# Performance work log

Hardware: AMD Instinct MI355X
Metric: run time of the kernel (lower is better)

## Reference

```python
import jax, jax.numpy as jnp
import numpy as np

N_QUERY, N_BACKGND, DIM = 2048, 8192, 32


def setup_inputs() -> dict:
    key = jax.random.key(0)
    k0, k1, k2, k3 = jax.random.split(key, 4)
    x_backgnd = jax.random.normal(k0, (N_BACKGND, DIM), dtype=jnp.float32)
    y_backgnd = jax.random.normal(k1, (N_BACKGND,), dtype=jnp.float32)
    x_query = jax.random.normal(k2, (N_QUERY, DIM), dtype=jnp.float32)
    r = jax.random.uniform(k3, (N_QUERY, N_BACKGND), dtype=jnp.float32)
    sigma = jnp.array([0.1], dtype=jnp.float32)      # nn.Parameter init_sigma
    r_scale = jnp.array([3.0], dtype=jnp.float32)    # nn.Parameter init_r_scale
    w = jnp.ones((DIM,), dtype=jnp.float32)          # trainable weights matrix
    return {"x_backgnd": x_backgnd, "y_backgnd": y_backgnd, "x_query": x_query,
            "r": r, "sigma": sigma, "r_scale": r_scale, "w": w}


def reference(x_backgnd, y_backgnd, x_query, r, sigma, r_scale, w):
    # weighted Euclidean distance: ||(xq - xb) * w|| via the expansion trick,
    # avoiding the (n_query, n_backgnd, dim) difference tensor.
    xq = x_query * w           # (nq, d)
    xb = x_backgnd * w         # (nb, d)
    q2 = jnp.sum(xq * xq, axis=1, keepdims=True)        # (nq, 1)
    b2 = jnp.sum(xb * xb, axis=1)                        # (nb,)
    d2 = q2 + b2[None, :] - 2.0 * (xq @ xb.T)            # (nq, nb)
    dists = jnp.sqrt(jnp.maximum(d2, 0.0))
    # exp kernel with relationship bias, normalize, weighted sum
    k_vals = jnp.exp(-dists / sigma + r_scale * r)       # sigma, r_scale broadcast (1,)
    k_sum = jnp.sum(k_vals, axis=1, keepdims=True) + 1e-8
    weights = k_vals / k_sum
    y_pred = weights @ y_backgnd                          # (nq,)
    return y_pred
```

## Files before the change

### kernel.cpp

```cpp
#include <hip/hip_runtime.h>
#include <math.h>

#define NQ 2048
#define NB 8192
#define DIM 32

#define LOG2E 1.44269504088896340736f

typedef _Float16 half8 __attribute__((ext_vector_type(8)));
typedef float    f32x4 __attribute__((ext_vector_type(4)));

#define WS_ACC 0
#define WS_Q2  16448
#define WS_B2  24640
#define WS_XQH 57408
#define WS_XBH 188480

__global__ __launch_bounds__(256) void relnw_pre(
    const float* __restrict__ xq, const float* __restrict__ xb,
    const float* __restrict__ w,
    _Float16* __restrict__ XQh, _Float16* __restrict__ XBh,
    float* __restrict__ q2, float* __restrict__ b2,
    float* __restrict__ acc)
{
    const int tid = threadIdx.x;
    const int gi  = blockIdx.x * 256 + tid;
    if (gi < 2 * NQ) acc[gi] = 0.f;

    const int row = blockIdx.x * 64 + (tid >> 2);
    const int p   = tid & 3;
    if (row >= NQ + NB) return;

    const float* src; _Float16* dst; float* s2; float scale;
    if (row < NQ) { src = xq + (size_t)row * DIM;
                    dst = XQh + (size_t)row * DIM; s2 = q2 + row; scale = 1.f; }
    else          { int j = row - NQ;
                    src = xb + (size_t)j * DIM;
                    dst = XBh + (size_t)j * DIM;   s2 = b2 + j;   scale = -2.f; }

    const float4 xa  = ((const float4*)src)[p * 2];
    const float4 xbv = ((const float4*)src)[p * 2 + 1];
    const float4 wa  = ((const float4*)w)[p * 2];
    const float4 wb  = ((const float4*)w)[p * 2 + 1];
    const float xs[8]  = {xa.x, xa.y, xa.z, xa.w, xbv.x, xbv.y, xbv.z, xbv.w};
    const float ws_[8] = {wa.x, wa.y, wa.z, wa.w, wb.x, wb.y, wb.z, wb.w};

    half8 h;
    float s = 0.f;
#pragma unroll
    for (int c = 0; c < 8; ++c) {
        float t = xs[c] * ws_[c];
        _Float16 hh = (_Float16)t;
        float th = (float)hh;
        s = fmaf(th, th, s);
        h[c] = (_Float16)(th * scale);
    }
    *(half8*)(dst + p * 8) = h;

    s += __shfl_xor(s, 1, 64);
    s += __shfl_xor(s, 2, 64);
    if (p == 0) *s2 = s;
}

#define BT_PER_WAVE 16
#define BG_PER_WAVE (BT_PER_WAVE * 16)

__global__ __launch_bounds__(256) void relnw_main(
    const _Float16* __restrict__ XQh,
    const _Float16* __restrict__ XBh,
    const float* __restrict__ q2,
    const float* __restrict__ b2,
    const float* __restrict__ yb,
    const float* __restrict__ r,
    const float* __restrict__ sigma,
    const float* __restrict__ rscale,
    float* __restrict__ acc)
{
    const int tid  = threadIdx.x;
    const int lane = tid & 63;
    const int wid  = tid >> 6;
    const int m    = lane & 15;
    const int quad = lane >> 4;

    const int q0     = blockIdx.y * 16;
    const int bstart = (blockIdx.x * 4 + wid) * BG_PER_WAVE;

    const float c1 = -LOG2E / sigma[0];
    const float c2 =  LOG2E * rscale[0];

    const half8 afrag = *(const half8*)(XQh + (size_t)(q0 + m) * DIM + quad * 8);

    float q2r[4];
#pragma unroll
    for (int g = 0; g < 4; ++g) q2r[g] = q2[q0 + quad * 4 + g];

    const _Float16* xbp = XBh + (size_t)(bstart + m) * DIM + quad * 8;
    const float*    rp  = r + (size_t)(q0 + quad * 4) * NB + bstart + m;

    float sk[4]  = {0.f, 0.f, 0.f, 0.f};
    float sky[4] = {0.f, 0.f, 0.f, 0.f};

#pragma unroll
    for (int it = 0; it < BT_PER_WAVE; ++it) {
        const int bc = bstart + it * 16 + m;
        const half8 bfrag = *(const half8*)(xbp + (size_t)it * 16 * DIM);
        const float yv  = yb[bc];
        const float b2v = b2[bc];
        float rr[4];
#pragma unroll
        for (int g = 0; g < 4; ++g) rr[g] = rp[(size_t)g * NB + it * 16];

        f32x4 cin;
#pragma unroll
        for (int g = 0; g < 4; ++g) cin[g] = q2r[g] + b2v;

        f32x4 d2v = __builtin_amdgcn_mfma_f32_16x16x32_f16(
            afrag, bfrag, cin, 0, 0, 0);

#pragma unroll
        for (int g = 0; g < 4; ++g) {
            float d2 = fmaxf(d2v[g], 0.f);
            float dist = __builtin_amdgcn_sqrtf(d2);
            float e = fmaf(dist, c1, rr[g] * c2);
            float k = __builtin_amdgcn_exp2f(e);
            sk[g] += k;
            sky[g] = fmaf(k, yv, sky[g]);
        }
    }

#pragma unroll
    for (int off = 1; off <= 8; off <<= 1) {
#pragma unroll
        for (int g = 0; g < 4; ++g) {
            sk[g]  += __shfl_xor(sk[g],  off, 64);
            sky[g] += __shfl_xor(sky[g], off, 64);
        }
    }
    if (m == 0) {
#pragma unroll
        for (int g = 0; g < 4; ++g) {
            atomicAdd(acc + (q0 + quad * 4 + g),      sk[g]);
            atomicAdd(acc + NQ + (q0 + quad * 4 + g), sky[g]);
        }
    }
}

__global__ __launch_bounds__(256) void relnw_finalize(
    const float* __restrict__ acc, float* __restrict__ out)
{
    int q = blockIdx.x * 256 + threadIdx.x;
    if (q < NQ)
        out[q] = acc[NQ + q] / (acc[q] + 1e-8f);
}

extern "C" void kernel_launch(void* const* d_in, const int* in_sizes, int n_in,
                              void* d_out, int out_size, void* d_ws, size_t ws_size,
                              hipStream_t stream) {
    const float* xb     = (const float*)d_in[0];
    const float* yb     = (const float*)d_in[1];
    const float* xq     = (const float*)d_in[2];
    const float* r      = (const float*)d_in[3];
    const float* sigma  = (const float*)d_in[4];
    const float* rscale = (const float*)d_in[5];
    const float* w      = (const float*)d_in[6];
    float* out = (float*)d_out;

    char* ws = (char*)d_ws;
    float*    acc = (float*)(ws + WS_ACC);
    float*    q2  = (float*)(ws + WS_Q2);
    float*    b2  = (float*)(ws + WS_B2);
    _Float16* XQh = (_Float16*)(ws + WS_XQH);
    _Float16* XBh = (_Float16*)(ws + WS_XBH);

    relnw_pre<<<(NQ + NB) / 64, 256, 0, stream>>>(xq, xb, w, XQh, XBh, q2, b2, acc);

    dim3 grid(NB / (4 * BG_PER_WAVE), NQ / 16);
    relnw_main<<<grid, 256, 0, stream>>>(XQh, XBh, q2, b2, yb, r, sigma, rscale, acc);

    relnw_finalize<<<(NQ + 255) / 256, 256, 0, stream>>>(acc, out);
}
```

Before: 112.8 us.

## Fuse preprocessing into main kernel and replace atomics with per-chunk partials

Removes the separate preprocessing kernel: the main kernel now reads fp32 query/background rows directly, applies the weights, converts to fp16 and computes the squared norms in-kernel, with b2 staged in shared memory. Global atomics are replaced by per-chunk partial sums written to the workspace and reduced in the finalize kernel, which also removes the need to zero the accumulator. This saves one launch and the fp16 workspace round trip, but every block recomputes background norms and reads fp32 background data (twice the bytes of fp16) redundantly across the 128 query blocks.

```diff
diff --git a/kernel.cpp b/kernel.cpp
--- a/kernel.cpp
+++ b/kernel.cpp
@@ -10,72 +10,26 @@
 typedef _Float16 half8 __attribute__((ext_vector_type(8)));
 typedef float    f32x4 __attribute__((ext_vector_type(4)));
 
-#define WS_ACC 0
-#define WS_Q2  16448
-#define WS_B2  24640
-#define WS_XQH 57408
-#define WS_XBH 188480
-
-__global__ __launch_bounds__(256) void relnw_pre(
-    const float* __restrict__ xq, const float* __restrict__ xb,
-    const float* __restrict__ w,
-    _Float16* __restrict__ XQh, _Float16* __restrict__ XBh,
-    float* __restrict__ q2, float* __restrict__ b2,
-    float* __restrict__ acc)
-{
-    const int tid = threadIdx.x;
-    const int gi  = blockIdx.x * 256 + tid;
-    if (gi < 2 * NQ) acc[gi] = 0.f;
-
-    const int row = blockIdx.x * 64 + (tid >> 2);
-    const int p   = tid & 3;
-    if (row >= NQ + NB) return;
-
-    const float* src; _Float16* dst; float* s2; float scale;
-    if (row < NQ) { src = xq + (size_t)row * DIM;
-                    dst = XQh + (size_t)row * DIM; s2 = q2 + row; scale = 1.f; }
-    else          { int j = row - NQ;
-                    src = xb + (size_t)j * DIM;
-                    dst = XBh + (size_t)j * DIM;   s2 = b2 + j;   scale = -2.f; }
-
-    const float4 xa  = ((const float4*)src)[p * 2];
-    const float4 xbv = ((const float4*)src)[p * 2 + 1];
-    const float4 wa  = ((const float4*)w)[p * 2];
-    const float4 wb  = ((const float4*)w)[p * 2 + 1];
-    const float xs[8]  = {xa.x, xa.y, xa.z, xa.w, xbv.x, xbv.y, xbv.z, xbv.w};
-    const float ws_[8] = {wa.x, wa.y, wa.z, wa.w, wb.x, wb.y, wb.z, wb.w};
-
-    half8 h;
-    float s = 0.f;
-#pragma unroll
-    for (int c = 0; c < 8; ++c) {
-        float t = xs[c] * ws_[c];
-        _Float16 hh = (_Float16)t;
-        float th = (float)hh;
-        s = fmaf(th, th, s);
-        h[c] = (_Float16)(th * scale);
-    }
-    *(half8*)(dst + p * 8) = h;
-
-    s += __shfl_xor(s, 1, 64);
-    s += __shfl_xor(s, 2, 64);
-    if (p == 0) *s2 = s;
-}
+#define NCHUNK 32
+#define WS_PSK  0
+#define WS_PSKY (NCHUNK * NQ * 4)
 
 #define BT_PER_WAVE 16
 #define BG_PER_WAVE (BT_PER_WAVE * 16)
 
 __global__ __launch_bounds__(256) void relnw_main(
-    const _Float16* __restrict__ XQh,
-    const _Float16* __restrict__ XBh,
-    const float* __restrict__ q2,
-    const float* __restrict__ b2,
+    const float* __restrict__ xb,
     const float* __restrict__ yb,
+    const float* __restrict__ xq,
     const float* __restrict__ r,
     const float* __restrict__ sigma,
     const float* __restrict__ rscale,
-    float* __restrict__ acc)
+    const float* __restrict__ w,
+    float* __restrict__ psk,
+    float* __restrict__ psky)
 {
+    __shared__ float b2l[4][BG_PER_WAVE];
+
     const int tid  = threadIdx.x;
     const int lane = tid & 63;
     const int wid  = tid >> 6;
@@ -83,19 +37,81 @@
     const int quad = lane >> 4;
 
     const int q0     = blockIdx.y * 16;
-    const int bstart = (blockIdx.x * 4 + wid) * BG_PER_WAVE;
+    const int chunk  = blockIdx.x * 4 + wid;
+    const int bstart = chunk * BG_PER_WAVE;
 
     const float c1 = -LOG2E / sigma[0];
     const float c2 =  LOG2E * rscale[0];
 
-    const half8 afrag = *(const half8*)(XQh + (size_t)(q0 + m) * DIM + quad * 8);
+    float wq[8], wc[8];
+    {
+        const float4 a = ((const float4*)(w + quad * 8))[0];
+        const float4 b = ((const float4*)(w + quad * 8))[1];
+        wq[0]=a.x; wq[1]=a.y; wq[2]=a.z; wq[3]=a.w;
+        wq[4]=b.x; wq[5]=b.y; wq[6]=b.z; wq[7]=b.w;
+        const int p = lane & 3;
+        const float4 c = ((const float4*)(w + p * 8))[0];
+        const float4 d = ((const float4*)(w + p * 8))[1];
+        wc[0]=c.x; wc[1]=c.y; wc[2]=c.z; wc[3]=c.w;
+        wc[4]=d.x; wc[5]=d.y; wc[6]=d.z; wc[7]=d.w;
+    }
+
+    half8 afrag;
+    {
+        const float* row = xq + (size_t)(q0 + m) * DIM + quad * 8;
+        const float4 a = ((const float4*)row)[0];
+        const float4 b = ((const float4*)row)[1];
+        const float v[8] = {a.x,a.y,a.z,a.w,b.x,b.y,b.z,b.w};
+#pragma unroll
+        for (int c = 0; c < 8; ++c) afrag[c] = (_Float16)(v[c] * wq[c]);
+    }
 
     float q2r[4];
-#pragma unroll
-    for (int g = 0; g < 4; ++g) q2r[g] = q2[q0 + quad * 4 + g];
-
-    const _Float16* xbp = XBh + (size_t)(bstart + m) * DIM + quad * 8;
-    const float*    rp  = r + (size_t)(q0 + quad * 4) * NB + bstart + m;
+    {
+        const int p = lane & 3, rw = lane >> 2;
+        const float* src = xq + (size_t)(q0 + rw) * DIM + p * 8;
+        const float4 a = ((const float4*)src)[0];
+        const float4 b = ((const float4*)src)[1];
+        const float v[8] = {a.x,a.y,a.z,a.w,b.x,b.y,b.z,b.w};
+        float s = 0.f;
+#pragma unroll
+        for (int c = 0; c < 8; ++c) {
+            float th = (float)(_Float16)(v[c] * wc[c]);
+            s = fmaf(th, th, s);
+        }
+        s += __shfl_xor(s, 1, 64);
+        s += __shfl_xor(s, 2, 64);
+#pragma unroll
+        for (int g = 0; g < 4; ++g)
+            q2r[g] = __shfl(s, (quad * 4 + g) * 4, 64);
+    }
+
+    {
+        const int p = lane & 3, rw = lane >> 2;
+#pragma unroll
+        for (int pass = 0; pass < BG_PER_WAVE / 16; ++pass) {
+            const int lrow = pass * 16 + rw;
+            const float* src = xb + (size_t)(bstart + lrow) * DIM + p * 8;
+            const float4 a = ((const float4*)src)[0];
+            const float4 b = ((const float4*)src)[1];
+            const float v[8] = {a.x,a.y,a.z,a.w,b.x,b.y,b.z,b.w};
+            float s = 0.f;
+#pragma unroll
+            for (int c = 0; c < 8; ++c) {
+                float th = (float)(_Float16)(v[c] * wc[c]);
+                s = fmaf(th, th, s);
+            }
+            s += __shfl_xor(s, 1, 64);
+            s += __shfl_xor(s, 2, 64);
+            if (p == 0) b2l[wid][lrow] = s;
+        }
+    }
+    __syncthreads();
+
+    const float* rbase[4];
+#pragma unroll
+    for (int g = 0; g < 4; ++g)
+        rbase[g] = r + (size_t)(q0 + quad * 4 + g) * NB + bstart + m;
 
     float sk[4]  = {0.f, 0.f, 0.f, 0.f};
     float sky[4] = {0.f, 0.f, 0.f, 0.f};
@@ -103,12 +119,20 @@
 #pragma unroll
     for (int it = 0; it < BT_PER_WAVE; ++it) {
         const int bc = bstart + it * 16 + m;
-        const half8 bfrag = *(const half8*)(xbp + (size_t)it * 16 * DIM);
+        const float* row = xb + (size_t)bc * DIM + quad * 8;
+        const float4 a = ((const float4*)row)[0];
+        const float4 b = ((const float4*)row)[1];
+        const float v[8] = {a.x,a.y,a.z,a.w,b.x,b.y,b.z,b.w};
+        half8 bfrag;
+#pragma unroll
+        for (int c = 0; c < 8; ++c)
+            bfrag[c] = (_Float16)(-2.0f) * (_Float16)(v[c] * wq[c]);
+
         const float yv  = yb[bc];
-        const float b2v = b2[bc];
+        const float b2v = b2l[wid][it * 16 + m];
         float rr[4];
 #pragma unroll
-        for (int g = 0; g < 4; ++g) rr[g] = rp[(size_t)g * NB + it * 16];
+        for (int g = 0; g < 4; ++g) rr[g] = rbase[g][it * 16];
 
         f32x4 cin;
 #pragma unroll
@@ -137,20 +161,25 @@
         }
     }
     if (m == 0) {
-#pragma unroll
-        for (int g = 0; g < 4; ++g) {
-            atomicAdd(acc + (q0 + quad * 4 + g),      sk[g]);
-            atomicAdd(acc + NQ + (q0 + quad * 4 + g), sky[g]);
-        }
+        f32x4 vk  = {sk[0],  sk[1],  sk[2],  sk[3]};
+        f32x4 vky = {sky[0], sky[1], sky[2], sky[3]};
+        *(f32x4*)(psk  + (size_t)chunk * NQ + q0 + quad * 4) = vk;
+        *(f32x4*)(psky + (size_t)chunk * NQ + q0 + quad * 4) = vky;
     }
 }
 
 __global__ __launch_bounds__(256) void relnw_finalize(
-    const float* __restrict__ acc, float* __restrict__ out)
+    const float* __restrict__ psk, const float* __restrict__ psky,
+    float* __restrict__ out)
 {
     int q = blockIdx.x * 256 + threadIdx.x;
-    if (q < NQ)
-        out[q] = acc[NQ + q] / (acc[q] + 1e-8f);
+    float sk = 0.f, sky = 0.f;
+#pragma unroll
+    for (int c = 0; c < NCHUNK; ++c) {
+        sk  += psk[(size_t)c * NQ + q];
+        sky += psky[(size_t)c * NQ + q];
+    }
+    out[q] = sky / (sk + 1e-8f);
 }
 
 extern "C" void kernel_launch(void* const* d_in, const int* in_sizes, int n_in,
@@ -166,16 +195,11 @@
     float* out = (float*)d_out;
 
     char* ws = (char*)d_ws;
-    float*    acc = (float*)(ws + WS_ACC);
-    float*    q2  = (float*)(ws + WS_Q2);
-    float*    b2  = (float*)(ws + WS_B2);
-    _Float16* XQh = (_Float16*)(ws + WS_XQH);
-    _Float16* XBh = (_Float16*)(ws + WS_XBH);
-
-    relnw_pre<<<(NQ + NB) / 64, 256, 0, stream>>>(xq, xb, w, XQh, XBh, q2, b2, acc);
+    float* psk  = (float*)(ws + WS_PSK);
+    float* psky = (float*)(ws + WS_PSKY);
 
     dim3 grid(NB / (4 * BG_PER_WAVE), NQ / 16);
-    relnw_main<<<grid, 256, 0, stream>>>(XQh, XBh, q2, b2, yb, r, sigma, rscale, acc);
-
-    relnw_finalize<<<(NQ + 255) / 256, 256, 0, stream>>>(acc, out);
+    relnw_main<<<grid, 256, 0, stream>>>(xb, yb, xq, r, sigma, rscale, w,
+                                         psk, psky);
+    relnw_finalize<<<NQ / 256, 256, 0, stream>>>(psk, psky, out);
 }
```

Result: slower. 130.6 us (+15.8%).

## Replace atomic accumulation with per-chunk partial sums and halve per-wave tile

Applied to the files above, without the earlier changes.

Each wave now writes its partial k-sum and k*y-sum for 16 queries into a per-chunk buffer, and the finalize kernel reduces those 64 chunks per query. This removes the float atomics and the zeroing of the accumulator in the prep kernel. The background range per wave is halved, which doubles the grid (and so the parallelism) while making each wave's loop shorter. In exchange, finalize reads about 1 MB of partials and the workspace grows. The r loads are also rewritten as four per-row base pointers.

```diff
diff --git a/kernel.cpp b/kernel.cpp
--- a/kernel.cpp
+++ b/kernel.cpp
@@ -10,23 +10,21 @@
 typedef _Float16 half8 __attribute__((ext_vector_type(8)));
 typedef float    f32x4 __attribute__((ext_vector_type(4)));
 
-#define WS_ACC 0
-#define WS_Q2  16448
-#define WS_B2  24640
-#define WS_XQH 57408
-#define WS_XBH 188480
+#define NCHUNK 64
+#define WS_PSK  0
+#define WS_PSKY (NCHUNK * NQ * 4)
+#define WS_Q2   (2 * NCHUNK * NQ * 4)
+#define WS_B2   (WS_Q2 + NQ * 4)
+#define WS_XQH  (WS_B2 + NB * 4)
+#define WS_XBH  (WS_XQH + NQ * DIM * 2)
 
 __global__ __launch_bounds__(256) void relnw_pre(
     const float* __restrict__ xq, const float* __restrict__ xb,
     const float* __restrict__ w,
     _Float16* __restrict__ XQh, _Float16* __restrict__ XBh,
-    float* __restrict__ q2, float* __restrict__ b2,
-    float* __restrict__ acc)
+    float* __restrict__ q2, float* __restrict__ b2)
 {
     const int tid = threadIdx.x;
-    const int gi  = blockIdx.x * 256 + tid;
-    if (gi < 2 * NQ) acc[gi] = 0.f;
-
     const int row = blockIdx.x * 64 + (tid >> 2);
     const int p   = tid & 3;
     if (row >= NQ + NB) return;
@@ -62,7 +60,7 @@
     if (p == 0) *s2 = s;
 }
 
-#define BT_PER_WAVE 16
+#define BT_PER_WAVE 8
 #define BG_PER_WAVE (BT_PER_WAVE * 16)
 
 __global__ __launch_bounds__(256) void relnw_main(
@@ -74,7 +72,8 @@
     const float* __restrict__ r,
     const float* __restrict__ sigma,
     const float* __restrict__ rscale,
-    float* __restrict__ acc)
+    float* __restrict__ psk,
+    float* __restrict__ psky)
 {
     const int tid  = threadIdx.x;
     const int lane = tid & 63;
@@ -83,7 +82,8 @@
     const int quad = lane >> 4;
 
     const int q0     = blockIdx.y * 16;
-    const int bstart = (blockIdx.x * 4 + wid) * BG_PER_WAVE;
+    const int chunk  = blockIdx.x * 4 + wid;
+    const int bstart = chunk * BG_PER_WAVE;
 
     const float c1 = -LOG2E / sigma[0];
     const float c2 =  LOG2E * rscale[0];
@@ -95,7 +95,11 @@
     for (int g = 0; g < 4; ++g) q2r[g] = q2[q0 + quad * 4 + g];
 
     const _Float16* xbp = XBh + (size_t)(bstart + m) * DIM + quad * 8;
-    const float*    rp  = r + (size_t)(q0 + quad * 4) * NB + bstart + m;
+
+    const float* rbase[4];
+#pragma unroll
+    for (int g = 0; g < 4; ++g)
+        rbase[g] = r + (size_t)(q0 + quad * 4 + g) * NB + bstart + m;
 
     float sk[4]  = {0.f, 0.f, 0.f, 0.f};
     float sky[4] = {0.f, 0.f, 0.f, 0.f};
@@ -108,7 +112,7 @@
         const float b2v = b2[bc];
         float rr[4];
 #pragma unroll
-        for (int g = 0; g < 4; ++g) rr[g] = rp[(size_t)g * NB + it * 16];
+        for (int g = 0; g < 4; ++g) rr[g] = rbase[g][it * 16];
 
         f32x4 cin;
 #pragma unroll
@@ -137,20 +141,25 @@
         }
     }
     if (m == 0) {
-#pragma unroll
-        for (int g = 0; g < 4; ++g) {
-            atomicAdd(acc + (q0 + quad * 4 + g),      sk[g]);
-            atomicAdd(acc + NQ + (q0 + quad * 4 + g), sky[g]);
-        }
+        f32x4 vk  = {sk[0],  sk[1],  sk[2],  sk[3]};
+        f32x4 vky = {sky[0], sky[1], sky[2], sky[3]};
+        *(f32x4*)(psk  + (size_t)chunk * NQ + q0 + quad * 4) = vk;
+        *(f32x4*)(psky + (size_t)chunk * NQ + q0 + quad * 4) = vky;
     }
 }
 
 __global__ __launch_bounds__(256) void relnw_finalize(
-    const float* __restrict__ acc, float* __restrict__ out)
+    const float* __restrict__ psk, const float* __restrict__ psky,
+    float* __restrict__ out)
 {
     int q = blockIdx.x * 256 + threadIdx.x;
-    if (q < NQ)
-        out[q] = acc[NQ + q] / (acc[q] + 1e-8f);
+    float sk = 0.f, sky = 0.f;
+#pragma unroll 8
+    for (int c = 0; c < NCHUNK; ++c) {
+        sk  += psk[(size_t)c * NQ + q];
+        sky += psky[(size_t)c * NQ + q];
+    }
+    out[q] = sky / (sk + 1e-8f);
 }
 
 extern "C" void kernel_launch(void* const* d_in, const int* in_sizes, int n_in,
@@ -166,16 +175,18 @@
     float* out = (float*)d_out;
 
     char* ws = (char*)d_ws;
-    float*    acc = (float*)(ws + WS_ACC);
-    float*    q2  = (float*)(ws + WS_Q2);
-    float*    b2  = (float*)(ws + WS_B2);
-    _Float16* XQh = (_Float16*)(ws + WS_XQH);
-    _Float16* XBh = (_Float16*)(ws + WS_XBH);
+    float*    psk  = (float*)(ws + WS_PSK);
+    float*    psky = (float*)(ws + WS_PSKY);
+    float*    q2   = (float*)(ws + WS_Q2);
+    float*    b2   = (float*)(ws + WS_B2);
+    _Float16* XQh  = (_Float16*)(ws + WS_XQH);
+    _Float16* XBh  = (_Float16*)(ws + WS_XBH);
 
-    relnw_pre<<<(NQ + NB) / 64, 256, 0, stream>>>(xq, xb, w, XQh, XBh, q2, b2, acc);
+    relnw_pre<<<(NQ + NB) / 64, 256, 0, stream>>>(xq, xb, w, XQh, XBh, q2, b2);
 
     dim3 grid(NB / (4 * BG_PER_WAVE), NQ / 16);
-    relnw_main<<<grid, 256, 0, stream>>>(XQh, XBh, q2, b2, yb, r, sigma, rscale, acc);
+    relnw_main<<<grid, 256, 0, stream>>>(XQh, XBh, q2, b2, yb, r, sigma, rscale,
+                                         psk, psky);
 
-    relnw_finalize<<<(NQ + 255) / 256, 256, 0, stream>>>(acc, out);
+    relnw_finalize<<<NQ / 256, 256, 0, stream>>>(psk, psky, out);
 }
```

Measured after the change: 116.4 us. 3.3% more time.
